# Optimization experiments

Hardware: AMD Instinct MI355X
Metric: run time of the kernel (lower is better)

The kernel has to match this reference:

```python
import jax, jax.numpy as jnp
import numpy as np

N = 100000   # nodes
E = 1600000  # edges (before self-loops)
IN = 128     # in_num
H1, C1 = 8, 8    # gat1: 8 heads x 8 channels -> 64 concat
OUT = 32     # out_num (gat2: 1 head x 32)


def setup_inputs() -> dict:
    key = jax.random.key(0)
    ks = jax.random.split(key, 10)
    g = lambda k, shape, fan: (jax.random.normal(k, shape, jnp.float32) / np.sqrt(fan).astype(np.float32))
    return {
        "x": jax.random.normal(ks[0], (N, IN), jnp.float32),
        "edge_index": jax.random.randint(ks[1], (2, E), 0, N, dtype=jnp.int64),
        "W1": g(ks[2], (IN, H1 * C1), IN),
        "a_src1": g(ks[3], (H1, C1), C1),
        "a_dst1": g(ks[4], (H1, C1), C1),
        "b1": jnp.zeros((H1 * C1,), jnp.float32),
        "W2": g(ks[5], (H1 * C1, OUT), H1 * C1),
        "a_src2": g(ks[6], (1, OUT), OUT),
        "a_dst2": g(ks[7], (1, OUT), OUT),
        "b2": jnp.zeros((OUT,), jnp.float32),
    }


def _gat_layer(x, src, dst, W, a_src, a_dst, b, heads, ch):
    # PyG GATConv (concat=True, negative_slope=0.2). Dropout (p=0.6) is a
    # no-op in eval mode and omitted.
    n = x.shape[0]
    h = (x @ W).reshape(n, heads, ch)                        # [N,H,C]
    al_s = jnp.einsum('nhc,hc->nh', h, a_src)                # [N,H]
    al_d = jnp.einsum('nhc,hc->nh', h, a_dst)
    e = jax.nn.leaky_relu(al_s[src] + al_d[dst], negative_slope=0.2)  # [E,H]
    # segment softmax over incoming edges of each dst node
    m = jax.lax.stop_gradient(jax.ops.segment_max(e, dst, num_segments=n))
    ex = jnp.exp(e - m[dst])
    denom = jax.ops.segment_sum(ex, dst, num_segments=n)
    alpha = ex / denom[dst]                                  # [E,H]
    out = jax.ops.segment_sum(h[src] * alpha[:, :, None], dst, num_segments=n)
    return out.reshape(n, heads * ch) + b


def reference(x, edge_index, W1, a_src1, a_dst1, b1, W2, a_src2, a_dst2, b2):
    loop = jnp.arange(N, dtype=edge_index.dtype)
    src = jnp.concatenate([edge_index[0], loop])  # add_self_loops=True (PyG default)
    dst = jnp.concatenate([edge_index[1], loop])
    h = _gat_layer(x, src, dst, W1, a_src1, a_dst1, b1, H1, C1)   # [N,64]
    out = _gat_layer(h, src, dst, W2, a_src2, a_dst2, b2, 1, OUT)  # [N,OUT]
    return out
```

## Files before the change

### kernel.cpp

```cpp
#include <hip/hip_runtime.h>
#include <hip/hip_bf16.h>


#define SLAB 8192

typedef float v2f __attribute__((ext_vector_type(2)));

__device__ __forceinline__ float lrelu02(float x) { return x > 0.f ? x : 0.2f * x; }

__device__ __forceinline__ unsigned short f2bf(float v) {
    __hip_bfloat16 b = __float2bfloat16(v);
    return __builtin_bit_cast(unsigned short, b);
}

__device__ __forceinline__ void accum8(uint4 hv, float ex, v2f* acc) {
    v2f ex2 = {ex, ex};
#pragma unroll
    for (int q = 0; q < 4; ++q) {
        unsigned u = (&hv.x)[q];
        v2f h2 = {__uint_as_float(u << 16), __uint_as_float(u & 0xffff0000u)};
        acc[q] = __builtin_elementwise_fma(h2, ex2, acc[q]);
    }
}

__device__ __forceinline__ v2f shfl_xor_v2(v2f v, int mask) {
    v2f r;
    r.x = __shfl_xor(v.x, mask, 64);
    r.y = __shfl_xor(v.y, mask, 64);
    return r;
}


__global__ __launch_bounds__(256)
void bucket_scatter_kernel(const int* __restrict__ ei, int e_real, int e_total,
                           unsigned M, int* __restrict__ bcur_pad,
                           int2* __restrict__ pairs) {
    __shared__ int cnt[256], loff[256], lcur[256], gbase[256];
    __shared__ int2 stag[4096];
    __shared__ unsigned short bb[4096];
    const int t = threadIdx.x;
    const int base = blockIdx.x * 4096;
    cnt[t] = 0;
    __syncthreads();

    int rs[16], rd[16], rb[16];
#pragma unroll
    for (int k = 0; k < 16; ++k) {
        int i = base + k * 256 + t;
        bool val = i < e_total;
        int s = 0, d = 0;
        if (val) {
            if (i < e_real) { s = ei[i]; d = ei[e_real + i]; }
            else            { s = d = i - e_real; }
        }
        int b = val ? (int)__umulhi((unsigned)d, M) : -1;
        rs[k] = s; rd[k] = d; rb[k] = b;
        if (val) atomicAdd(&cnt[b], 1);
    }
    __syncthreads();

    loff[t] = cnt[t];
    __syncthreads();
    for (int off = 1; off < 256; off <<= 1) {
        int v = (t >= off) ? loff[t - off] : 0;
        __syncthreads();
        loff[t] += v;
        __syncthreads();
    }
    int excl = loff[t] - cnt[t];
    __syncthreads();
    loff[t] = excl;
    lcur[t] = excl;
    gbase[t] = t * SLAB + atomicAdd(&bcur_pad[t * 16], cnt[t]);
    __syncthreads();

#pragma unroll
    for (int k = 0; k < 16; ++k) {
        if (rb[k] >= 0) {
            int lp = atomicAdd(&lcur[rb[k]], 1);
            stag[lp] = make_int2(rs[k], rd[k]);
            bb[lp]   = (unsigned short)rb[k];
        }
    }
    __syncthreads();

    int cn = e_total - base; if (cn > 4096) cn = 4096;
    for (int idx = t; idx < cn; idx += 256) {
        int b = bb[idx];
        int g = gbase[b] + (idx - loff[b]);
        pairs[g] = stag[idx];
    }
}

__global__ __launch_bounds__(256)
void csr_finalize_kernel(const int2* __restrict__ pairs,
                         const int* __restrict__ bcur_pad,
                         unsigned M, int n,
                         int* __restrict__ offsets,
                         int* __restrict__ srcs) {
    const int b = blockIdx.x;
    const int t = threadIdx.x;
    const unsigned long long Mll = M;
    int lo = (int)((((unsigned long long)b << 32) + Mll - 1) / Mll);
    int hi = (int)((((unsigned long long)(b + 1) << 32) + Mll - 1) / Mll);
    if (lo > n) lo = n;
    if (hi > n) hi = n;
    const int R    = hi - lo;
    const int cntb = bcur_pad[b * 16];
    const int2* sp = pairs + (size_t)b * SLAB;

    __shared__ int bs[256];
    __shared__ int ebeg_s;
    bs[t] = bcur_pad[t * 16];
    __syncthreads();
    for (int off = 1; off < 256; off <<= 1) {
        int v = (t >= off) ? bs[t - off] : 0;
        __syncthreads();
        bs[t] += v;
        __syncthreads();
    }
    if (t == 0) ebeg_s = (b == 0) ? 0 : bs[b - 1];
    __syncthreads();
    const int ebeg = ebeg_s;
    if (b == 255 && t == 0) offsets[n] = bs[255];

    __shared__ int deg[512], sc[512], cur[512];
    deg[t] = 0; deg[t + 256] = 0;
    __syncthreads();
    for (int j = t; j < cntb; j += 256)
        atomicAdd(&deg[sp[j].y - lo], 1);
    __syncthreads();

    sc[t] = deg[t]; sc[t + 256] = deg[t + 256];
    __syncthreads();
    for (int off = 1; off < 512; off <<= 1) {
        int v0 = (t >= off) ? sc[t - off] : 0;
        int v1 = (t + 256 >= off) ? sc[t + 256 - off] : 0;
        __syncthreads();
        sc[t] += v0; sc[t + 256] += v1;
        __syncthreads();
    }
    int e0 = sc[t] - deg[t];
    int e1 = sc[t + 256] - deg[t + 256];
    cur[t] = e0; cur[t + 256] = e1;
    if (t < R)       offsets[lo + t]       = ebeg + e0;
    if (t + 256 < R) offsets[lo + t + 256] = ebeg + e1;
    __syncthreads();

    for (int j = t; j < cntb; j += 256) {
        int2 p = sp[j];
        int pos = atomicAdd(&cur[p.y - lo], 1);
        srcs[ebeg + pos] = p.x;
    }
}

template<int K, int OUTC, int H, int C, int NPT, int KCHUNK>
__global__ __launch_bounds__(256)
void gemm_al_kernel(const float* __restrict__ x,
                    const float* __restrict__ W,
                    const float* __restrict__ a_src,
                    const float* __restrict__ a_dst,
                    unsigned short* __restrict__ h,
                    float* __restrict__ al_s,
                    float* __restrict__ al_d,
                    int n) {
    constexpr int COLG = OUTC / 4;
    constexpr int NG   = 256 / COLG;
    static_assert(NG * 8 == NPT, "tile mismatch");
    constexpr int LDX  = KCHUNK + 1;
    __shared__ float Xs[NPT * LDX];
    __shared__ float Ws[KCHUNK * OUTC];

    const int t    = threadIdx.x;
    const int mg   = t / COLG;
    const int cg   = t % COLG;
    const int base = blockIdx.x * NPT;

    float acc[8][4];
#pragma unroll
    for (int i = 0; i < 8; ++i)
#pragma unroll
        for (int j = 0; j < 4; ++j) acc[i][j] = 0.f;

    for (int kc = 0; kc < K; kc += KCHUNK) {
        __syncthreads();
        constexpr int F4R = KCHUNK / 4;
        constexpr int TOTF4 = NPT * F4R;
#pragma unroll
        for (int r = 0; r < TOTF4 / 256; ++r) {
            int f4   = r * 256 + t;
            int node = f4 / F4R;
            int kq   = f4 % F4R;
            int gn   = base + node; if (gn > n - 1) gn = n - 1;
            const float4 v = *(const float4*)&x[(size_t)gn * K + kc + kq * 4];
            float* d = &Xs[node * LDX + kq * 4];
            d[0] = v.x; d[1] = v.y; d[2] = v.z; d[3] = v.w;
        }
        constexpr int WF4 = KCHUNK * OUTC / 4;
        for (int idx = t; idx < WF4; idx += 256)
            *(float4*)&Ws[idx * 4] = *(const float4*)&W[(size_t)kc * OUTC + idx * 4];
        __syncthreads();

#pragma unroll 4
        for (int k = 0; k < KCHUNK; ++k) {
            float4 b = *(const float4*)&Ws[k * OUTC + cg * 4];
            float a[8];
#pragma unroll
            for (int i = 0; i < 8; ++i) a[i] = Xs[(mg * 8 + i) * LDX + k];
#pragma unroll
            for (int i = 0; i < 8; ++i) {
                acc[i][0] += a[i] * b.x;
                acc[i][1] += a[i] * b.y;
                acc[i][2] += a[i] * b.z;
                acc[i][3] += a[i] * b.w;
            }
        }
    }

    const float4 as4 = *(const float4*)&a_src[cg * 4];
    const float4 ad4 = *(const float4*)&a_dst[cg * 4];
    constexpr int GPH = C / 4;
    const int head = cg / GPH;
#pragma unroll
    for (int i = 0; i < 8; ++i) {
        int gn = base + mg * 8 + i;
        bool ok = gn < n;
        if (ok) {
            ushort4 hv;
            hv.x = f2bf(acc[i][0]); hv.y = f2bf(acc[i][1]);
            hv.z = f2bf(acc[i][2]); hv.w = f2bf(acc[i][3]);
            *(ushort4*)&h[(size_t)gn * OUTC + cg * 4] = hv;
        }
        float ps = acc[i][0] * as4.x + acc[i][1] * as4.y +
                   acc[i][2] * as4.z + acc[i][3] * as4.w;
        float pd = acc[i][0] * ad4.x + acc[i][1] * ad4.y +
                   acc[i][2] * ad4.z + acc[i][3] * ad4.w;
#pragma unroll
        for (int s = 1; s < GPH; s <<= 1) {
            ps += __shfl_xor(ps, s, 64);
            pd += __shfl_xor(pd, s, 64);
        }
        if (ok && (cg % GPH) == 0) {
            al_s[(size_t)gn * H + head] = ps;
            al_d[(size_t)gn * H + head] = pd;
        }
    }
}

template<int H, int C>
__global__ __launch_bounds__(256)
void gat_agg_kernel(const int* __restrict__ offsets,
                    const int* __restrict__ srcs,
                    const float* __restrict__ al_s,
                    const float* __restrict__ al_d,
                    const unsigned short* __restrict__ hfeat,
                    const float* __restrict__ bias,
                    float* __restrict__ out, int n) {
    constexpr int OUTC = H * C;
    constexpr int CG   = OUTC / 8;
    constexpr int ES   = 64 / CG;
    const int wid  = (int)((blockIdx.x * blockDim.x + threadIdx.x) >> 6);
    const int lane = threadIdx.x & 63;
    const int cg   = lane % CG;
    const int es   = lane / CG;
    if (wid >= n) return;
    const int head = (cg * 8) / C;

    const float aldv = al_d[(size_t)wid * H + head];
    const int beg = offsets[wid];
    const int end = offsets[wid + 1];
    const int deg = end - beg;

    v2f acc[4];
#pragma unroll
    for (int q = 0; q < 4; ++q) acc[q] = (v2f){0.f, 0.f};
    float dsum = 0.f;

    if (deg <= ES) {
        int j = beg + es;
        bool v = j < end;
        int s = __builtin_nontemporal_load(&srcs[v ? j : beg]);
        const uint4 hv = *(const uint4*)&hfeat[(size_t)s * OUTC + cg * 8];
        float ls = al_s[(size_t)s * H + head];
        float ex = v ? __expf(lrelu02(ls + aldv)) : 0.f;
        accum8(hv, ex, acc);
        dsum += ex;
    } else if (deg <= 2 * ES) {
        int sA = __builtin_nontemporal_load(&srcs[beg + es]);
        int jB = beg + ES + es;
        bool vB = jB < end;
        int sB = __builtin_nontemporal_load(&srcs[vB ? jB : beg]);
        const uint4 hvA = *(const uint4*)&hfeat[(size_t)sA * OUTC + cg * 8];
        const uint4 hvB = *(const uint4*)&hfeat[(size_t)sB * OUTC + cg * 8];
        float lsA = al_s[(size_t)sA * H + head];
        float lsB = al_s[(size_t)sB * H + head];
        float exA = __expf(lrelu02(lsA + aldv));
        float exB = vB ? __expf(lrelu02(lsB + aldv)) : 0.f;
        accum8(hvA, exA, acc);
        accum8(hvB, exB, acc);
        dsum += exA + exB;
    } else if (deg <= 4 * ES) {
        int sA = __builtin_nontemporal_load(&srcs[beg + es]);
        int sB = __builtin_nontemporal_load(&srcs[beg + ES + es]);
        int jC = beg + 2 * ES + es;
        int jD = beg + 3 * ES + es;
        bool vC = jC < end;
        bool vD = jD < end;
        int sC = __builtin_nontemporal_load(&srcs[vC ? jC : beg]);
        int sD = __builtin_nontemporal_load(&srcs[vD ? jD : beg]);
        const uint4 hvA = *(const uint4*)&hfeat[(size_t)sA * OUTC + cg * 8];
        const uint4 hvB = *(const uint4*)&hfeat[(size_t)sB * OUTC + cg * 8];
        const uint4 hvC = *(const uint4*)&hfeat[(size_t)sC * OUTC + cg * 8];
        const uint4 hvD = *(const uint4*)&hfeat[(size_t)sD * OUTC + cg * 8];
        float lsA = al_s[(size_t)sA * H + head];
        float lsB = al_s[(size_t)sB * H + head];
        float lsC = al_s[(size_t)sC * H + head];
        float lsD = al_s[(size_t)sD * H + head];
        float exA = __expf(lrelu02(lsA + aldv));
        float exB = __expf(lrelu02(lsB + aldv));
        float exC = vC ? __expf(lrelu02(lsC + aldv)) : 0.f;
        float exD = vD ? __expf(lrelu02(lsD + aldv)) : 0.f;
        accum8(hvA, exA, acc);
        accum8(hvB, exB, acc);
        accum8(hvC, exC, acc);
        accum8(hvD, exD, acc);
        dsum += (exA + exB) + (exC + exD);
    } else {
        for (int j0 = beg; j0 < end; j0 += 2 * ES) {
            int jA = j0 + es;
            int jB = j0 + ES + es;
            bool vA = jA < end;
            bool vB = jB < end;
            int sA = __builtin_nontemporal_load(&srcs[vA ? jA : beg]);
            int sB = __builtin_nontemporal_load(&srcs[vB ? jB : beg]);
            const uint4 hvA = *(const uint4*)&hfeat[(size_t)sA * OUTC + cg * 8];
            const uint4 hvB = *(const uint4*)&hfeat[(size_t)sB * OUTC + cg * 8];
            float lsA = al_s[(size_t)sA * H + head];
            float lsB = al_s[(size_t)sB * H + head];
            float exA = vA ? __expf(lrelu02(lsA + aldv)) : 0.f;
            float exB = vB ? __expf(lrelu02(lsB + aldv)) : 0.f;
            accum8(hvA, exA, acc);
            accum8(hvB, exB, acc);
            dsum += exA + exB;
        }
    }

#pragma unroll
    for (int sh = CG; sh < 64; sh <<= 1) {
        dsum += __shfl_xor(dsum, sh, 64);
#pragma unroll
        for (int q = 0; q < 4; ++q) acc[q] += shfl_xor_v2(acc[q], sh);
    }

    if (es == 0) {
        float inv = 1.f / dsum;
        const float4 b0 = *(const float4*)&bias[cg * 8];
        const float4 b1 = *(const float4*)&bias[cg * 8 + 4];
        float4 o0, o1;
        o0.x = acc[0].x * inv + b0.x;
        o0.y = acc[0].y * inv + b0.y;
        o0.z = acc[1].x * inv + b0.z;
        o0.w = acc[1].y * inv + b0.w;
        o1.x = acc[2].x * inv + b1.x;
        o1.y = acc[2].y * inv + b1.y;
        o1.z = acc[3].x * inv + b1.z;
        o1.w = acc[3].y * inv + b1.w;
        *(float4*)&out[(size_t)wid * OUTC + cg * 8]     = o0;
        *(float4*)&out[(size_t)wid * OUTC + cg * 8 + 4] = o1;
    }
}


extern "C" void kernel_launch(void* const* d_in, const int* in_sizes, int n_in,
                              void* d_out, int out_size, void* d_ws, size_t ws_size,
                              hipStream_t stream) {
    const float* x   = (const float*)d_in[0];
    const int*   ei  = (const int*)  d_in[1];
    const float* W1  = (const float*)d_in[2];
    const float* as1 = (const float*)d_in[3];
    const float* ad1 = (const float*)d_in[4];
    const float* b1  = (const float*)d_in[5];
    const float* W2  = (const float*)d_in[6];
    const float* as2 = (const float*)d_in[7];
    const float* ad2 = (const float*)d_in[8];
    const float* b2  = (const float*)d_in[9];
    float* out = (float*)d_out;

    const int n       = in_sizes[0] / 128;
    const int e_real  = in_sizes[1] / 2;
    const int e_total = e_real + n;
    const unsigned M256 = (unsigned)((256ull << 32) / (unsigned)n);

    unsigned short* h1u = (unsigned short*)d_ws;
    float* fws  = (float*)d_ws;
    float* als1 = fws  + (size_t)n * 32;
    float* ald1 = als1 + (size_t)n * 8;
    float* agg1 = ald1 + (size_t)n * 8;
    int2*  pairs = (int2*)agg1;
    int* offsets  = (int*)(agg1 + (size_t)n * 64);
    int* srcs     = offsets + (n + 1);
    int* bcur_pad = srcs + e_total;

    hipMemsetAsync(bcur_pad, 0, 256 * 16 * sizeof(int), stream);
    bucket_scatter_kernel<<<(e_total + 4095) / 4096, 256, 0, stream>>>(
        ei, e_real, e_total, M256, bcur_pad, pairs);
    csr_finalize_kernel<<<256, 256, 0, stream>>>(pairs, bcur_pad, M256, n,
                                                 offsets, srcs);

    gemm_al_kernel<128, 64, 8, 8, 128, 64><<<(n + 127) / 128, 256, 0, stream>>>(
        x, W1, as1, ad1, h1u, als1, ald1, n);
    gat_agg_kernel<8, 8><<<(n + 3) / 4, 256, 0, stream>>>(
        offsets, srcs, als1, ald1, h1u, b1, agg1, n);

    gemm_al_kernel<64, 32, 1, 32, 256, 32><<<(n + 255) / 256, 256, 0, stream>>>(
        agg1, W2, as2, ad2, h1u, als1, ald1, n);
    gat_agg_kernel<1, 32><<<(n + 3) / 4, 256, 0, stream>>>(
        offsets, srcs, als1, ald1, h1u, b2, out, n);
}
```

Measured before the change: 278.1 us.

## Fuse edge bucket scatter with layer-1 GEMM and use 512 CSR buckets

Merges the edge bucket-scatter kernel and the first-layer GEMM/attention-logit kernel into one launch, with blocks choosing their role by block index, so the two independent phases share the GPU and one launch is removed. The bucket count goes from 256 to 512 with smaller slabs, so each finalize block handles about 196 nodes and 256 threads cover them with single-element scans. The fused kernel reserves about 49 KB of shared memory for every block, which may lower occupancy for the scatter blocks. The smaller slabs also leave less headroom if a bucket is heavily skewed.

```diff
diff --git a/kernel.cpp b/kernel.cpp
--- a/kernel.cpp
+++ b/kernel.cpp
@@ -2,7 +2,8 @@
 #include <hip/hip_bf16.h>
 
 
-#define SLAB 8192
+#define SLAB  4096
+#define NBUCK 512
 
 typedef float v2f __attribute__((ext_vector_type(2)));
 
@@ -30,17 +31,21 @@
     return r;
 }
 
-
-__global__ __launch_bounds__(256)
-void bucket_scatter_kernel(const int* __restrict__ ei, int e_real, int e_total,
-                           unsigned M, int* __restrict__ bcur_pad,
-                           int2* __restrict__ pairs) {
-    __shared__ int cnt[256], loff[256], lcur[256], gbase[256];
-    __shared__ int2 stag[4096];
-    __shared__ unsigned short bb[4096];
+__device__ __forceinline__ void scatter_body(char* smem, int vbid,
+                                             const int* __restrict__ ei,
+                                             int e_real, int e_total, unsigned M,
+                                             int* __restrict__ bcur_pad,
+                                             int2* __restrict__ pairs) {
+    int*  cnt   = (int*)smem;
+    int*  loff  = cnt + 512;
+    int*  lcur  = loff + 512;
+    int*  gbase = lcur + 512;
+    int2* stag  = (int2*)(gbase + 512);
+    unsigned short* bb = (unsigned short*)(stag + 4096);
+
     const int t = threadIdx.x;
-    const int base = blockIdx.x * 4096;
-    cnt[t] = 0;
+    const int base = vbid * 4096;
+    cnt[t] = 0; cnt[t + 256] = 0;
     __syncthreads();
 
     int rs[16], rd[16], rb[16];
@@ -59,19 +64,22 @@
     }
     __syncthreads();
 
-    loff[t] = cnt[t];
-    __syncthreads();
-    for (int off = 1; off < 256; off <<= 1) {
-        int v = (t >= off) ? loff[t - off] : 0;
-        __syncthreads();
-        loff[t] += v;
-        __syncthreads();
-    }
-    int excl = loff[t] - cnt[t];
-    __syncthreads();
-    loff[t] = excl;
-    lcur[t] = excl;
-    gbase[t] = t * SLAB + atomicAdd(&bcur_pad[t * 16], cnt[t]);
+    loff[t] = cnt[t]; loff[t + 256] = cnt[t + 256];
+    __syncthreads();
+    for (int off = 1; off < 512; off <<= 1) {
+        int v0 = (t >= off) ? loff[t - off] : 0;
+        int v1 = (t + 256 >= off) ? loff[t + 256 - off] : 0;
+        __syncthreads();
+        loff[t] += v0; loff[t + 256] += v1;
+        __syncthreads();
+    }
+    int e0 = loff[t] - cnt[t];
+    int e1 = loff[t + 256] - cnt[t + 256];
+    loff[t] = e0;           loff[t + 256] = e1;
+    lcur[t] = e0;           lcur[t + 256] = e1;
+    gbase[t]       = t * SLAB         + atomicAdd(&bcur_pad[t * 16], cnt[t]);
+    gbase[t + 256] = (t + 256) * SLAB + atomicAdd(&bcur_pad[(t + 256) * 16],
+                                                  cnt[t + 256]);
     __syncthreads();
 
 #pragma unroll
@@ -90,6 +98,129 @@
         int g = gbase[b] + (idx - loff[b]);
         pairs[g] = stag[idx];
     }
+}
+
+template<int K, int OUTC, int H, int C, int NPT, int KCHUNK>
+__device__ __forceinline__ void gemm_al_body(char* smem, int vbid,
+                                             const float* __restrict__ x,
+                                             const float* __restrict__ W,
+                                             const float* __restrict__ a_src,
+                                             const float* __restrict__ a_dst,
+                                             unsigned short* __restrict__ h,
+                                             float* __restrict__ al_s,
+                                             float* __restrict__ al_d,
+                                             int n) {
+    constexpr int COLG = OUTC / 4;
+    constexpr int NG   = 256 / COLG;
+    static_assert(NG * 8 == NPT, "tile mismatch");
+    constexpr int LDX  = KCHUNK + 1;
+    float* Xs = (float*)smem;
+    float* Ws = Xs + NPT * LDX;
+
+    const int t    = threadIdx.x;
+    const int mg   = t / COLG;
+    const int cg   = t % COLG;
+    const int base = vbid * NPT;
+
+    float acc[8][4];
+#pragma unroll
+    for (int i = 0; i < 8; ++i)
+#pragma unroll
+        for (int j = 0; j < 4; ++j) acc[i][j] = 0.f;
+
+    for (int kc = 0; kc < K; kc += KCHUNK) {
+        __syncthreads();
+        constexpr int F4R = KCHUNK / 4;
+        constexpr int TOTF4 = NPT * F4R;
+#pragma unroll
+        for (int r = 0; r < TOTF4 / 256; ++r) {
+            int f4   = r * 256 + t;
+            int node = f4 / F4R;
+            int kq   = f4 % F4R;
+            int gn   = base + node; if (gn > n - 1) gn = n - 1;
+            const float4 v = *(const float4*)&x[(size_t)gn * K + kc + kq * 4];
+            float* d = &Xs[node * LDX + kq * 4];
+            d[0] = v.x; d[1] = v.y; d[2] = v.z; d[3] = v.w;
+        }
+        constexpr int WF4 = KCHUNK * OUTC / 4;
+        for (int idx = t; idx < WF4; idx += 256)
+            *(float4*)&Ws[idx * 4] = *(const float4*)&W[(size_t)kc * OUTC + idx * 4];
+        __syncthreads();
+
+#pragma unroll 4
+        for (int k = 0; k < KCHUNK; ++k) {
+            float4 b = *(const float4*)&Ws[k * OUTC + cg * 4];
+            float a[8];
+#pragma unroll
+            for (int i = 0; i < 8; ++i) a[i] = Xs[(mg * 8 + i) * LDX + k];
+#pragma unroll
+            for (int i = 0; i < 8; ++i) {
+                acc[i][0] += a[i] * b.x;
+                acc[i][1] += a[i] * b.y;
+                acc[i][2] += a[i] * b.z;
+                acc[i][3] += a[i] * b.w;
+            }
+        }
+    }
+
+    const float4 as4 = *(const float4*)&a_src[cg * 4];
+    const float4 ad4 = *(const float4*)&a_dst[cg * 4];
+    constexpr int GPH = C / 4;
+    const int head = cg / GPH;
+#pragma unroll
+    for (int i = 0; i < 8; ++i) {
+        int gn = base + mg * 8 + i;
+        bool ok = gn < n;
+        if (ok) {
+            ushort4 hv;
+            hv.x = f2bf(acc[i][0]); hv.y = f2bf(acc[i][1]);
+            hv.z = f2bf(acc[i][2]); hv.w = f2bf(acc[i][3]);
+            *(ushort4*)&h[(size_t)gn * OUTC + cg * 4] = hv;
+        }
+        float ps = acc[i][0] * as4.x + acc[i][1] * as4.y +
+                   acc[i][2] * as4.z + acc[i][3] * as4.w;
+        float pd = acc[i][0] * ad4.x + acc[i][1] * ad4.y +
+                   acc[i][2] * ad4.z + acc[i][3] * ad4.w;
+#pragma unroll
+        for (int s = 1; s < GPH; s <<= 1) {
+            ps += __shfl_xor(ps, s, 64);
+            pd += __shfl_xor(pd, s, 64);
+        }
+        if (ok && (cg % GPH) == 0) {
+            al_s[(size_t)gn * H + head] = ps;
+            al_d[(size_t)gn * H + head] = pd;
+        }
+    }
+}
+
+__global__ __launch_bounds__(256)
+void scatter_gemm_kernel(const int* __restrict__ ei, int e_real, int e_total,
+                         unsigned M, int* __restrict__ bcur_pad,
+                         int2* __restrict__ pairs, int ns,
+                         const float* __restrict__ x,
+                         const float* __restrict__ W1,
+                         const float* __restrict__ as1,
+                         const float* __restrict__ ad1,
+                         unsigned short* __restrict__ h,
+                         float* __restrict__ al_s,
+                         float* __restrict__ al_d, int n) {
+    __shared__ __align__(16) char smem[49664];
+    if ((int)blockIdx.x < ns)
+        scatter_body(smem, blockIdx.x, ei, e_real, e_total, M, bcur_pad, pairs);
+    else
+        gemm_al_body<128, 64, 8, 8, 128, 64>(smem, blockIdx.x - ns,
+                                             x, W1, as1, ad1, h, al_s, al_d, n);
+}
+
+template<int K, int OUTC, int H, int C, int NPT, int KCHUNK>
+__global__ __launch_bounds__(256)
+void gemm_al_kernel(const float* __restrict__ x, const float* __restrict__ W,
+                    const float* __restrict__ a_src, const float* __restrict__ a_dst,
+                    unsigned short* __restrict__ h, float* __restrict__ al_s,
+                    float* __restrict__ al_d, int n) {
+    __shared__ __align__(16) char smem[(NPT * (KCHUNK + 1) + KCHUNK * OUTC) * 4];
+    gemm_al_body<K, OUTC, H, C, NPT, KCHUNK>(smem, blockIdx.x, x, W, a_src,
+                                             a_dst, h, al_s, al_d, n);
 }
 
 __global__ __launch_bounds__(256)
@@ -109,141 +240,47 @@
     const int cntb = bcur_pad[b * 16];
     const int2* sp = pairs + (size_t)b * SLAB;
 
-    __shared__ int bs[256];
+    __shared__ int bs[NBUCK];
     __shared__ int ebeg_s;
     bs[t] = bcur_pad[t * 16];
-    __syncthreads();
-    for (int off = 1; off < 256; off <<= 1) {
-        int v = (t >= off) ? bs[t - off] : 0;
-        __syncthreads();
-        bs[t] += v;
+    bs[t + 256] = bcur_pad[(t + 256) * 16];
+    __syncthreads();
+    for (int off = 1; off < NBUCK; off <<= 1) {
+        int v0 = (t >= off) ? bs[t - off] : 0;
+        int v1 = (t + 256 >= off) ? bs[t + 256 - off] : 0;
+        __syncthreads();
+        bs[t] += v0; bs[t + 256] += v1;
         __syncthreads();
     }
     if (t == 0) ebeg_s = (b == 0) ? 0 : bs[b - 1];
+    if (b == NBUCK - 1 && t == 0) offsets[n] = bs[NBUCK - 1];
     __syncthreads();
     const int ebeg = ebeg_s;
-    if (b == 255 && t == 0) offsets[n] = bs[255];
-
-    __shared__ int deg[512], sc[512], cur[512];
-    deg[t] = 0; deg[t + 256] = 0;
+
+    __shared__ int deg[256], sc[256], cur[256];
+    deg[t] = 0;
     __syncthreads();
     for (int j = t; j < cntb; j += 256)
         atomicAdd(&deg[sp[j].y - lo], 1);
     __syncthreads();
 
-    sc[t] = deg[t]; sc[t + 256] = deg[t + 256];
-    __syncthreads();
-    for (int off = 1; off < 512; off <<= 1) {
-        int v0 = (t >= off) ? sc[t - off] : 0;
-        int v1 = (t + 256 >= off) ? sc[t + 256 - off] : 0;
-        __syncthreads();
-        sc[t] += v0; sc[t + 256] += v1;
+    sc[t] = deg[t];
+    __syncthreads();
+    for (int off = 1; off < 256; off <<= 1) {
+        int v = (t >= off) ? sc[t - off] : 0;
+        __syncthreads();
+        sc[t] += v;
         __syncthreads();
     }
     int e0 = sc[t] - deg[t];
-    int e1 = sc[t + 256] - deg[t + 256];
-    cur[t] = e0; cur[t + 256] = e1;
-    if (t < R)       offsets[lo + t]       = ebeg + e0;
-    if (t + 256 < R) offsets[lo + t + 256] = ebeg + e1;
+    cur[t] = e0;
+    if (t < R) offsets[lo + t] = ebeg + e0;
     __syncthreads();
 
     for (int j = t; j < cntb; j += 256) {
         int2 p = sp[j];
         int pos = atomicAdd(&cur[p.y - lo], 1);
         srcs[ebeg + pos] = p.x;
-    }
-}
-
-template<int K, int OUTC, int H, int C, int NPT, int KCHUNK>
-__global__ __launch_bounds__(256)
-void gemm_al_kernel(const float* __restrict__ x,
-                    const float* __restrict__ W,
-                    const float* __restrict__ a_src,
-                    const float* __restrict__ a_dst,
-                    unsigned short* __restrict__ h,
-                    float* __restrict__ al_s,
-                    float* __restrict__ al_d,
-                    int n) {
-    constexpr int COLG = OUTC / 4;
-    constexpr int NG   = 256 / COLG;
-    static_assert(NG * 8 == NPT, "tile mismatch");
-    constexpr int LDX  = KCHUNK + 1;
-    __shared__ float Xs[NPT * LDX];
-    __shared__ float Ws[KCHUNK * OUTC];
-
-    const int t    = threadIdx.x;
-    const int mg   = t / COLG;
-    const int cg   = t % COLG;
-    const int base = blockIdx.x * NPT;
-
-    float acc[8][4];
-#pragma unroll
-    for (int i = 0; i < 8; ++i)
-#pragma unroll
-        for (int j = 0; j < 4; ++j) acc[i][j] = 0.f;
-
-    for (int kc = 0; kc < K; kc += KCHUNK) {
-        __syncthreads();
-        constexpr int F4R = KCHUNK / 4;
-        constexpr int TOTF4 = NPT * F4R;
-#pragma unroll
-        for (int r = 0; r < TOTF4 / 256; ++r) {
-            int f4   = r * 256 + t;
-            int node = f4 / F4R;
-            int kq   = f4 % F4R;
-            int gn   = base + node; if (gn > n - 1) gn = n - 1;
-            const float4 v = *(const float4*)&x[(size_t)gn * K + kc + kq * 4];
-            float* d = &Xs[node * LDX + kq * 4];
-            d[0] = v.x; d[1] = v.y; d[2] = v.z; d[3] = v.w;
-        }
-        constexpr int WF4 = KCHUNK * OUTC / 4;
-        for (int idx = t; idx < WF4; idx += 256)
-            *(float4*)&Ws[idx * 4] = *(const float4*)&W[(size_t)kc * OUTC + idx * 4];
-        __syncthreads();
-
-#pragma unroll 4
-        for (int k = 0; k < KCHUNK; ++k) {
-            float4 b = *(const float4*)&Ws[k * OUTC + cg * 4];
-            float a[8];
-#pragma unroll
-            for (int i = 0; i < 8; ++i) a[i] = Xs[(mg * 8 + i) * LDX + k];
-#pragma unroll
-            for (int i = 0; i < 8; ++i) {
-                acc[i][0] += a[i] * b.x;
-                acc[i][1] += a[i] * b.y;
-                acc[i][2] += a[i] * b.z;
-                acc[i][3] += a[i] * b.w;
-            }
-        }
-    }
-
-    const float4 as4 = *(const float4*)&a_src[cg * 4];
-    const float4 ad4 = *(const float4*)&a_dst[cg * 4];
-    constexpr int GPH = C / 4;
-    const int head = cg / GPH;
-#pragma unroll
-    for (int i = 0; i < 8; ++i) {
-        int gn = base + mg * 8 + i;
-        bool ok = gn < n;
-        if (ok) {
-            ushort4 hv;
-            hv.x = f2bf(acc[i][0]); hv.y = f2bf(acc[i][1]);
-            hv.z = f2bf(acc[i][2]); hv.w = f2bf(acc[i][3]);
-            *(ushort4*)&h[(size_t)gn * OUTC + cg * 4] = hv;
-        }
-        float ps = acc[i][0] * as4.x + acc[i][1] * as4.y +
-                   acc[i][2] * as4.z + acc[i][3] * as4.w;
-        float pd = acc[i][0] * ad4.x + acc[i][1] * ad4.y +
-                   acc[i][2] * ad4.z + acc[i][3] * ad4.w;
-#pragma unroll
-        for (int s = 1; s < GPH; s <<= 1) {
-            ps += __shfl_xor(ps, s, 64);
-            pd += __shfl_xor(pd, s, 64);
-        }
-        if (ok && (cg % GPH) == 0) {
-            al_s[(size_t)gn * H + head] = ps;
-            al_d[(size_t)gn * H + head] = pd;
-        }
     }
 }
 
@@ -389,7 +426,7 @@
     const int n       = in_sizes[0] / 128;
     const int e_real  = in_sizes[1] / 2;
     const int e_total = e_real + n;
-    const unsigned M256 = (unsigned)((256ull << 32) / (unsigned)n);
+    const unsigned M512 = (unsigned)(((unsigned long long)NBUCK << 32) / (unsigned)n);
 
     unsigned short* h1u = (unsigned short*)d_ws;
     float* fws  = (float*)d_ws;
@@ -401,14 +438,16 @@
     int* srcs     = offsets + (n + 1);
     int* bcur_pad = srcs + e_total;
 
-    hipMemsetAsync(bcur_pad, 0, 256 * 16 * sizeof(int), stream);
-    bucket_scatter_kernel<<<(e_total + 4095) / 4096, 256, 0, stream>>>(
-        ei, e_real, e_total, M256, bcur_pad, pairs);
-    csr_finalize_kernel<<<256, 256, 0, stream>>>(pairs, bcur_pad, M256, n,
-                                                 offsets, srcs);
-
-    gemm_al_kernel<128, 64, 8, 8, 128, 64><<<(n + 127) / 128, 256, 0, stream>>>(
+    const int ns = (e_total + 4095) / 4096;
+    const int g1 = (n + 127) / 128;
+
+    hipMemsetAsync(bcur_pad, 0, NBUCK * 16 * sizeof(int), stream);
+    scatter_gemm_kernel<<<ns + g1, 256, 0, stream>>>(
+        ei, e_real, e_total, M512, bcur_pad, pairs, ns,
         x, W1, as1, ad1, h1u, als1, ald1, n);
+    csr_finalize_kernel<<<NBUCK, 256, 0, stream>>>(pairs, bcur_pad, M512, n,
+                                                   offsets, srcs);
+
     gat_agg_kernel<8, 8><<<(n + 3) / 4, 256, 0, stream>>>(
         offsets, srcs, als1, ald1, h1u, b1, agg1, n);
 
```

New measurement: 270.0 us. 2.9% less time.
